# Performance work log

Hardware: AMD Instinct MI355X
Metric: run time of the kernel (lower is better)

## Reference

```python
import jax, jax.numpy as jnp
import numpy as np

TOP_K = 2
SCALING = 16.0 / 8.0  # alpha / rank


def setup_inputs() -> dict:
    key = jax.random.key(0)
    ks = jax.random.split(key, 9)
    B, V, D, P = 32, 21, 512, 64
    IN, OUT, E, R, H = D * P, 96, 8, 8, 256
    return {
        "x": jax.random.normal(ks[0], (B, V, D, P), jnp.float32),
        "W_base": jax.random.normal(ks[1], (OUT, IN), jnp.float32) * (IN ** -0.5),
        "b_base": jax.random.normal(ks[2], (OUT,), jnp.float32) * 0.01,
        "W1": jax.random.normal(ks[3], (H, D), jnp.float32) * (D ** -0.5),
        "b1": jax.random.normal(ks[4], (H,), jnp.float32) * 0.01,
        "W2": jax.random.normal(ks[5], (E, H), jnp.float32) * (H ** -0.5),
        "b2": jax.random.normal(ks[6], (E,), jnp.float32) * 0.01,
        "lora_A": jax.random.normal(ks[7], (E, R, IN), jnp.float32) * (IN ** -0.5),
        "lora_B": jax.random.normal(ks[8], (E, OUT, R), jnp.float32) * (R ** -0.5),
    }


def reference(x, W_base, b_base, W1, b1, W2, b2, lora_A, lora_B):
    B, V, D, P = x.shape
    E = lora_A.shape[0]
    # FlattenHead: flatten last two dims, then linear (dropout is identity in eval)
    flat = x.reshape(B, V, D * P)                      # [B, V, IN]
    base_out = flat @ W_base.T + b_base                # [B, V, OUT]
    # Router: pool over n_vars then patch dim -> [B, D]
    pooled = x.mean(axis=1).mean(axis=-1)
    h = jax.nn.relu(pooled @ W1.T + b1)
    logits = h @ W2.T + b2                             # [B, E]
    probs = jax.nn.softmax(logits, axis=-1)
    topw, topi = jax.lax.top_k(probs, TOP_K)           # [B, K]
    topw = topw / jnp.clip(topw.sum(-1, keepdims=True), 1e-6)
    # All LoRA experts (matches original dense compute), then weighted combine
    temp = jnp.einsum("bvi,eri->ebvr", flat, lora_A)   # [E, B, V, R]
    delta = jnp.einsum("ebvr,eor->ebvo", temp, lora_B) * SCALING  # [E, B, V, OUT]
    # Scatter top-k weights into dense [B, E] then combine (top-k sparse combine)
    w_full = jnp.zeros((B, E), x.dtype).at[jnp.arange(B)[:, None], topi].add(topw)
    moe_delta = jnp.einsum("be,ebvo->bvo", w_full, delta)
    return base_out + moe_delta, probs
```

## Files before the change

kernel.cpp:

```cpp
#include <hip/hip_runtime.h>

#define B_DIM 32
#define V_DIM 21
#define D_DIM 512
#define P_DIM 64
#define M_TOTAL 672
#define K_TOTAL 32768
#define OUT_DIM 96
#define E_DIM 8
#define R_DIM 8
#define H_DIM 256
#define N_TOTAL 160
#define SCALING 2.0f
#define POOL_SCALE (1.0f / (V_DIM * (float)P_DIM))

#define BM 64
#define BK 32
#define KSPLIT 64
#define K_PER_SPLIT (K_TOTAL / KSPLIT)
#define CHUNKS (K_PER_SPLIT / BK)
#define SMN (M_TOTAL * N_TOTAL)
#define RC_ROWS 2

typedef __attribute__((ext_vector_type(4))) float floatx4;
typedef __attribute__((ext_vector_type(8))) short short8;

__device__ __forceinline__ unsigned short f2bf(float f) {
  union { float f; unsigned int u; } v; v.f = f;
  unsigned int u = v.u + (0x7FFFu + ((v.u >> 16) & 1u));
  return (unsigned short)(u >> 16);
}

__device__ __forceinline__ unsigned int cvt_pk_bf16(float lo, float hi) {
  unsigned int r;
  asm("v_cvt_pk_bf16_f32 %0, %1, %2" : "=v"(r) : "v"(lo), "v"(hi));
  return r;
}

__device__ __forceinline__ void gl_lds16(const void* g, void* l) {
  __builtin_amdgcn_global_load_lds(
      (const __attribute__((address_space(1))) void*)g,
      (__attribute__((address_space(3))) void*)l, 16, 0, 0);
}

__global__ __launch_bounds__(256)
void convW_kernel(const float* __restrict__ W_base, const float* __restrict__ lora_A,
                  short* __restrict__ Wb, float* __restrict__ pooled) {
  int gid = blockIdx.x * 256 + threadIdx.x;
  if (blockIdx.x < 64) pooled[gid] = 0.0f;
  size_t base = (size_t)gid * 8;
  int row = (int)(base >> 15);
  int k = (int)(base & 32767);
  const float* src = (row < OUT_DIM) ? (W_base + ((size_t)row << 15) + k)
                                     : (lora_A + ((size_t)(row - OUT_DIM) << 15) + k);
  floatx4 v0 = ((const floatx4*)src)[0];
  floatx4 v1 = ((const floatx4*)src)[1];
  short8 sv;
  sv[0] = (short)f2bf(v0[0]); sv[1] = (short)f2bf(v0[1]);
  sv[2] = (short)f2bf(v0[2]); sv[3] = (short)f2bf(v0[3]);
  sv[4] = (short)f2bf(v1[0]); sv[5] = (short)f2bf(v1[1]);
  sv[6] = (short)f2bf(v1[2]); sv[7] = (short)f2bf(v1[3]);
  *(short8*)(Wb + base) = sv;
}

__global__ __launch_bounds__(256, 4)
void gemm_kernel(const float* __restrict__ x, const short* __restrict__ Wb,
                 float* __restrict__ P, float* __restrict__ pooled) {
  __shared__ __attribute__((aligned(16))) float ldsA[2][BM * BK];
  __shared__ __attribute__((aligned(16))) short ldsB[2][N_TOTAL * BK];
  __shared__ float lds_pool[5 * 8];

  const int tid = threadIdx.x;
  const int m0 = blockIdx.x * BM;
  const int ky = blockIdx.y;
  const int kbase = ky * K_PER_SPLIT;
  const int lane = tid & 63;
  const int wave = tid >> 6;
  const int quad = lane >> 4;
  const int l16 = lane & 15;
  const int b_first = m0 / V_DIM;
  const int d_first = kbase >> 6;

  if (tid < 40) lds_pool[tid] = 0.0f;

  const float* srcA[2];
  int dstA[2];
  #pragma unroll
  for (int it = 0; it < 2; ++it) {
    int idx = it * 256 + tid;
    int row = idx >> 3, j = idx & 7;
    int m = m0 + row; if (m > M_TOTAL - 1) m = M_TOTAL - 1;
    srcA[it] = x + (size_t)m * K_TOTAL + kbase + ((j ^ (row & 7)) << 2);
    dstA[it] = (it * 256 + (tid & 192)) << 2;
  }
  const short* srcB[3];
  int dstB[3];
  #pragma unroll
  for (int it = 0; it < 3; ++it) {
    int idx = it * 256 + tid;
    if (idx < 640) {
      int pair = idx >> 3, s8 = idx & 7;
      int c8 = s8 ^ (pair & 7);
      int row = pair * 2 + (c8 >> 2), j = c8 & 3;
      srcB[it] = Wb + (size_t)row * K_TOTAL + kbase + (j << 3);
      dstB[it] = (it * 256 + (tid & 192)) << 3;
    } else {
      srcB[it] = Wb; dstB[it] = 0;
    }
  }

  const int prow = tid >> 2;
  const int part = tid & 3;
  const int ps1 = (prow + part) & 7;
  const int ps2 = (ps1 + 4) & 7;
  const int pm = m0 + prow;
  const int pool_base = (pm < M_TOTAL) ? ((pm / V_DIM) - b_first) * 8 : -1;

#define ISSUE(c, bb)                                                          \
  {                                                                           \
    _Pragma("unroll")                                                         \
    for (int it = 0; it < 2; ++it)                                            \
      gl_lds16(srcA[it] + (c) * BK, &ldsA[bb][dstA[it]]);                     \
    _Pragma("unroll")                                                         \
    for (int it = 0; it < 2; ++it)                                            \
      gl_lds16(srcB[it] + (c) * BK, &ldsB[bb][dstB[it]]);                     \
    if (tid < 128) gl_lds16(srcB[2] + (c) * BK, &ldsB[bb][dstB[2]]);          \
  }

  floatx4 acc[10];
  #pragma unroll
  for (int nt = 0; nt < 10; ++nt) acc[nt] = (floatx4)(0.0f);

  ISSUE(0, 0);
  __syncthreads();

  #pragma unroll
  for (int c = 0; c < CHUNKS; ++c) {
    const int buf = c & 1;
    if (c + 1 < CHUNKS) ISSUE(c + 1, buf ^ 1);
    {
      const floatx4* aT = (const floatx4*)ldsA[buf];
      floatx4 u = aT[prow * 8 + ps1];
      floatx4 w = aT[prow * 8 + ps2];
      float s = ((u[0] + u[1]) + (u[2] + u[3])) + ((w[0] + w[1]) + (w[2] + w[3]));
      s += __shfl_down(s, 2, 4);
      s += __shfl_down(s, 1, 4);
      if (part == 0 && pool_base >= 0)
        atomicAdd(&lds_pool[pool_base + (c >> 1)], s);
    }
    {
      const floatx4* aT = (const floatx4*)ldsA[buf];
      const int r = wave * 16 + l16;
      floatx4 f0 = aT[r * 8 + ((2 * quad) ^ (r & 7))];
      floatx4 f1 = aT[r * 8 + ((2 * quad + 1) ^ (r & 7))];
      union { short8 s; unsigned int u[4]; } av;
      av.u[0] = cvt_pk_bf16(f0[0], f0[1]);
      av.u[1] = cvt_pk_bf16(f0[2], f0[3]);
      av.u[2] = cvt_pk_bf16(f1[0], f1[1]);
      av.u[3] = cvt_pk_bf16(f1[2], f1[3]);
      const short8* bT = (const short8*)ldsB[buf];
      #pragma unroll
      for (int nt = 0; nt < 10; ++nt) {
        int r2 = nt * 16 + l16;
        int pr = r2 >> 1;
        short8 b = bT[pr * 8 + ((((r2 & 1) << 2) | quad) ^ (pr & 7))];
        acc[nt] = __builtin_amdgcn_mfma_f32_16x16x32_bf16(av.s, b, acc[nt], 0, 0, 0);
      }
    }
    __syncthreads();
  }

  {
    const int mrow = m0 + wave * 16 + quad * 4;
    float* Pp = P + (size_t)ky * SMN + (size_t)mrow * N_TOTAL + l16;
    #pragma unroll
    for (int r = 0; r < 4; ++r)
      if (mrow + r < M_TOTAL)
        #pragma unroll
        for (int nt = 0; nt < 10; ++nt)
          Pp[(size_t)r * N_TOTAL + nt * 16] = acc[nt][r];
  }

  if (tid < 40) {
    int b = b_first + (tid >> 3);
    int d = d_first + (tid & 7);
    if (b < B_DIM)
      atomicAdd(&pooled[b * D_DIM + d], lds_pool[tid] * POOL_SCALE);
  }
}

__global__ __launch_bounds__(256)
void router_kernel(const float* __restrict__ pooled, const float* __restrict__ W1,
                   const float* __restrict__ b1, const float* __restrict__ W2,
                   const float* __restrict__ b2, float* __restrict__ wfull,
                   float* __restrict__ probs_out) {
  __shared__ float sp[D_DIM];
  __shared__ float sh[H_DIM];
  __shared__ float slog[E_DIM];
  const int b = blockIdx.x;
  const int t = threadIdx.x;
  sp[t] = pooled[b * D_DIM + t];
  sp[t + 256] = pooled[b * D_DIM + t + 256];
  __syncthreads();
  float acc = b1[t];
  const float* w1r = W1 + (size_t)t * D_DIM;
  for (int d = 0; d < D_DIM; ++d) acc += sp[d] * w1r[d];
  sh[t] = fmaxf(acc, 0.0f);
  __syncthreads();
  if (t < E_DIM) {
    float a = b2[t];
    const float* w2r = W2 + t * H_DIM;
    for (int j = 0; j < H_DIM; ++j) a += sh[j] * w2r[j];
    slog[t] = a;
  }
  __syncthreads();
  if (t == 0) {
    float p[E_DIM];
    float mx = slog[0];
    for (int e = 1; e < E_DIM; ++e) mx = fmaxf(mx, slog[e]);
    float se = 0.0f;
    for (int e = 0; e < E_DIM; ++e) { p[e] = __expf(slog[e] - mx); se += p[e]; }
    float inv = 1.0f / se;
    for (int e = 0; e < E_DIM; ++e) { p[e] *= inv; probs_out[b * E_DIM + e] = p[e]; }
    int i0 = 0;
    for (int e = 1; e < E_DIM; ++e) if (p[e] > p[i0]) i0 = e;
    int i1 = (i0 == 0) ? 1 : 0;
    for (int e = 0; e < E_DIM; ++e) if (e != i0 && p[e] > p[i1]) i1 = e;
    float s2 = p[i0] + p[i1];
    float invs = 1.0f / fmaxf(s2, 1e-6f);
    for (int e = 0; e < E_DIM; ++e) {
      float w = 0.0f;
      if (e == i0) w += p[i0] * invs;
      if (e == i1) w += p[i1] * invs;
      wfull[b * E_DIM + e] = w;
    }
  }
}

__global__ __launch_bounds__(256)
void reduce_combine_kernel(const float* __restrict__ P, const float* __restrict__ b_base,
                           const float* __restrict__ lora_B, const float* __restrict__ wfull,
                           float* __restrict__ out) {
  __shared__ float sS[RC_ROWS * N_TOTAL];
  const int t = threadIdx.x;
  const size_t base = (size_t)blockIdx.x * (RC_ROWS * N_TOTAL);
  for (int s = t; s < RC_ROWS * N_TOTAL; s += 256) {
    const float* Pp = P + base + s;
    float a = 0.0f;
    #pragma unroll 8
    for (int k = 0; k < KSPLIT; ++k) a += Pp[(size_t)k * SMN];
    sS[s] = a;
  }
  __syncthreads();
  if (t < RC_ROWS * OUT_DIM) {
    int mr = t / OUT_DIM;
    int o = t - mr * OUT_DIM;
    int mm = blockIdx.x * RC_ROWS + mr;
    int b = mm / V_DIM;
    const float* srow = sS + mr * N_TOTAL;
    float res = srow[o] + b_base[o];
    float moe = 0.0f;
    #pragma unroll
    for (int e = 0; e < E_DIM; ++e) {
      float we = wfull[b * E_DIM + e];
      if (we != 0.0f) {
        const float* lb = lora_B + ((size_t)e * OUT_DIM + o) * R_DIM;
        float dd = 0.0f;
        #pragma unroll
        for (int r = 0; r < R_DIM; ++r) dd += srow[OUT_DIM + e * R_DIM + r] * lb[r];
        moe += we * dd;
      }
    }
    out[(size_t)mm * OUT_DIM + o] = res + SCALING * moe;
  }
}

extern "C" void kernel_launch(void* const* d_in, const int* in_sizes, int n_in,
                              void* d_out, int out_size, void* d_ws, size_t ws_size,
                              hipStream_t stream) {
  const float* x      = (const float*)d_in[0];
  const float* W_base = (const float*)d_in[1];
  const float* b_base = (const float*)d_in[2];
  const float* W1     = (const float*)d_in[3];
  const float* b1     = (const float*)d_in[4];
  const float* W2     = (const float*)d_in[5];
  const float* b2     = (const float*)d_in[6];
  const float* lora_A = (const float*)d_in[7];
  const float* lora_B = (const float*)d_in[8];
  float* out = (float*)d_out;

  float* ws     = (float*)d_ws;
  float* pooled = ws;
  float* wfull  = ws + 16384;
  short* Wb     = (short*)(wfull + 256);
  float* P      = (float*)(Wb + (size_t)N_TOTAL * K_TOTAL);

  convW_kernel<<<(N_TOTAL * K_TOTAL / 8 + 255) / 256, 256, 0, stream>>>(
      W_base, lora_A, Wb, pooled);
  gemm_kernel<<<dim3(11, KSPLIT), 256, 0, stream>>>(x, Wb, P, pooled);
  router_kernel<<<B_DIM, 256, 0, stream>>>(pooled, W1, b1, W2, b2, wfull,
                                           out + (size_t)M_TOTAL * OUT_DIM);
  reduce_combine_kernel<<<M_TOTAL / RC_ROWS, 256, 0, stream>>>(
      P, b_base, lora_B, wfull, out);
}
```

Baseline: 206.1 us.

## Fuse weight bf16 conversion into GEMM, halve K-split, drop pooled atomics

Removes the separate weight-conversion kernel: the GEMM now loads fp32 W_base/lora_A rows into registers, converts them to bf16 and writes them to LDS after the MFMA work of each chunk. KSPLIT drops from 64 to 32, which halves the partial-sum buffer and the reduce traffic. Pooled sums are written as per-block partials and combined in the router instead of using global atomics, so no zeroing is needed. The reduce kernel is vectorised with float4 loads. The trade-offs are that each M-block now re-reads and re-converts fp32 weights (twice the bytes of the bf16 copy, repeated across 11 M-blocks), fewer GEMM blocks are launched, and register pressure rises.

```diff
diff --git a/kernel.cpp b/kernel.cpp
--- a/kernel.cpp
+++ b/kernel.cpp
@@ -16,20 +16,16 @@
 
 #define BM 64
 #define BK 32
-#define KSPLIT 64
+#define KSPLIT 32
 #define K_PER_SPLIT (K_TOTAL / KSPLIT)
 #define CHUNKS (K_PER_SPLIT / BK)
 #define SMN (M_TOTAL * N_TOTAL)
-#define RC_ROWS 2
+#define NMB 11
+#define RC_ROWS 4
 
 typedef __attribute__((ext_vector_type(4))) float floatx4;
 typedef __attribute__((ext_vector_type(8))) short short8;
-
-__device__ __forceinline__ unsigned short f2bf(float f) {
-  union { float f; unsigned int u; } v; v.f = f;
-  unsigned int u = v.u + (0x7FFFu + ((v.u >> 16) & 1u));
-  return (unsigned short)(u >> 16);
-}
+typedef __attribute__((ext_vector_type(2))) unsigned int uintx2;
 
 __device__ __forceinline__ unsigned int cvt_pk_bf16(float lo, float hi) {
   unsigned int r;
@@ -43,35 +39,17 @@
       (__attribute__((address_space(3))) void*)l, 16, 0, 0);
 }
 
-__global__ __launch_bounds__(256)
-void convW_kernel(const float* __restrict__ W_base, const float* __restrict__ lora_A,
-                  short* __restrict__ Wb, float* __restrict__ pooled) {
-  int gid = blockIdx.x * 256 + threadIdx.x;
-  if (blockIdx.x < 64) pooled[gid] = 0.0f;
-  size_t base = (size_t)gid * 8;
-  int row = (int)(base >> 15);
-  int k = (int)(base & 32767);
-  const float* src = (row < OUT_DIM) ? (W_base + ((size_t)row << 15) + k)
-                                     : (lora_A + ((size_t)(row - OUT_DIM) << 15) + k);
-  floatx4 v0 = ((const floatx4*)src)[0];
-  floatx4 v1 = ((const floatx4*)src)[1];
-  short8 sv;
-  sv[0] = (short)f2bf(v0[0]); sv[1] = (short)f2bf(v0[1]);
-  sv[2] = (short)f2bf(v0[2]); sv[3] = (short)f2bf(v0[3]);
-  sv[4] = (short)f2bf(v1[0]); sv[5] = (short)f2bf(v1[1]);
-  sv[6] = (short)f2bf(v1[2]); sv[7] = (short)f2bf(v1[3]);
-  *(short8*)(Wb + base) = sv;
-}
-
 __global__ __launch_bounds__(256, 4)
-void gemm_kernel(const float* __restrict__ x, const short* __restrict__ Wb,
-                 float* __restrict__ P, float* __restrict__ pooled) {
+void gemm_kernel(const float* __restrict__ x, const float* __restrict__ W_base,
+                 const float* __restrict__ lora_A, float* __restrict__ P,
+                 float* __restrict__ pp) {
   __shared__ __attribute__((aligned(16))) float ldsA[2][BM * BK];
   __shared__ __attribute__((aligned(16))) short ldsB[2][N_TOTAL * BK];
-  __shared__ float lds_pool[5 * 8];
+  __shared__ float lds_pool[5 * 16];
 
   const int tid = threadIdx.x;
-  const int m0 = blockIdx.x * BM;
+  const int mb = blockIdx.x;
+  const int m0 = mb * BM;
   const int ky = blockIdx.y;
   const int kbase = ky * K_PER_SPLIT;
   const int lane = tid & 63;
@@ -79,12 +57,11 @@
   const int quad = lane >> 4;
   const int l16 = lane & 15;
   const int b_first = m0 / V_DIM;
-  const int d_first = kbase >> 6;
-
-  if (tid < 40) lds_pool[tid] = 0.0f;
-
-  const float* srcA[2];
-  int dstA[2];
+  const int d_first = ky * (K_PER_SPLIT / P_DIM);
+
+  if (tid < 80) lds_pool[tid] = 0.0f;
+
+  const float* srcA[2]; int dstA[2];
   #pragma unroll
   for (int it = 0; it < 2; ++it) {
     int idx = it * 256 + tid;
@@ -93,20 +70,19 @@
     srcA[it] = x + (size_t)m * K_TOTAL + kbase + ((j ^ (row & 7)) << 2);
     dstA[it] = (it * 256 + (tid & 192)) << 2;
   }
-  const short* srcB[3];
-  int dstB[3];
+
+  const float* srcB[5]; int offB[5];
   #pragma unroll
-  for (int it = 0; it < 3; ++it) {
+  for (int it = 0; it < 5; ++it) {
     int idx = it * 256 + tid;
-    if (idx < 640) {
-      int pair = idx >> 3, s8 = idx & 7;
-      int c8 = s8 ^ (pair & 7);
-      int row = pair * 2 + (c8 >> 2), j = c8 & 3;
-      srcB[it] = Wb + (size_t)row * K_TOTAL + kbase + (j << 3);
-      dstB[it] = (it * 256 + (tid & 192)) << 3;
-    } else {
-      srcB[it] = Wb; dstB[it] = 0;
-    }
+    int row = idx >> 3, j = idx & 7;
+    const float* wrow = (row < OUT_DIM)
+        ? (W_base + (size_t)row * K_TOTAL)
+        : (lora_A + (size_t)(row - OUT_DIM) * K_TOTAL);
+    srcB[it] = wrow + kbase + (j << 2);
+    int p = row >> 1;
+    int c8 = ((row & 1) << 2) | (j >> 1);
+    offB[it] = p * 64 + ((c8 ^ (p & 7)) << 3) + ((j & 1) << 2);
   }
 
   const int prow = tid >> 2;
@@ -114,30 +90,37 @@
   const int ps1 = (prow + part) & 7;
   const int ps2 = (ps1 + 4) & 7;
   const int pm = m0 + prow;
-  const int pool_base = (pm < M_TOTAL) ? ((pm / V_DIM) - b_first) * 8 : -1;
-
-#define ISSUE(c, bb)                                                          \
-  {                                                                           \
-    _Pragma("unroll")                                                         \
-    for (int it = 0; it < 2; ++it)                                            \
-      gl_lds16(srcA[it] + (c) * BK, &ldsA[bb][dstA[it]]);                     \
-    _Pragma("unroll")                                                         \
-    for (int it = 0; it < 2; ++it)                                            \
-      gl_lds16(srcB[it] + (c) * BK, &ldsB[bb][dstB[it]]);                     \
-    if (tid < 128) gl_lds16(srcB[2] + (c) * BK, &ldsB[bb][dstB[2]]);          \
-  }
-
+  const int pool_base = (pm < M_TOTAL) ? ((pm / V_DIM) - b_first) * 16 : -1;
+
+  floatx4 rb[5];
   floatx4 acc[10];
   #pragma unroll
   for (int nt = 0; nt < 10; ++nt) acc[nt] = (floatx4)(0.0f);
 
-  ISSUE(0, 0);
-  __syncthreads();
-
-  #pragma unroll
+#define BLOAD(c)                                                              \
+  { _Pragma("unroll")                                                         \
+    for (int it = 0; it < 5; ++it)                                            \
+      rb[it] = *(const floatx4*)(srcB[it] + (c) * BK); }
+#define AISSUE(c, bb)                                                         \
+  { _Pragma("unroll")                                                         \
+    for (int it = 0; it < 2; ++it)                                            \
+      gl_lds16(srcA[it] + (c) * BK, &ldsA[bb][dstA[it]]); }
+#define BWRITE(bb)                                                            \
+  { _Pragma("unroll")                                                         \
+    for (int it = 0; it < 5; ++it) {                                          \
+      uintx2 w;                                                               \
+      w[0] = cvt_pk_bf16(rb[it][0], rb[it][1]);                               \
+      w[1] = cvt_pk_bf16(rb[it][2], rb[it][3]);                               \
+      *(uintx2*)&ldsB[bb][offB[it]] = w;                                      \
+    } }
+
+  BLOAD(0); AISSUE(0, 0); BWRITE(0);
+  __syncthreads();
+
+  #pragma unroll 2
   for (int c = 0; c < CHUNKS; ++c) {
     const int buf = c & 1;
-    if (c + 1 < CHUNKS) ISSUE(c + 1, buf ^ 1);
+    if (c + 1 < CHUNKS) { BLOAD(c + 1); AISSUE(c + 1, buf ^ 1); }
     {
       const floatx4* aT = (const floatx4*)ldsA[buf];
       floatx4 u = aT[prow * 8 + ps1];
@@ -167,6 +150,7 @@
         acc[nt] = __builtin_amdgcn_mfma_f32_16x16x32_bf16(av.s, b, acc[nt], 0, 0, 0);
       }
     }
+    if (c + 1 < CHUNKS) BWRITE(buf ^ 1);
     __syncthreads();
   }
 
@@ -181,16 +165,14 @@
           Pp[(size_t)r * N_TOTAL + nt * 16] = acc[nt][r];
   }
 
-  if (tid < 40) {
-    int b = b_first + (tid >> 3);
-    int d = d_first + (tid & 7);
-    if (b < B_DIM)
-      atomicAdd(&pooled[b * D_DIM + d], lds_pool[tid] * POOL_SCALE);
+  if (tid < 80) {
+    int bl = tid >> 4, dl = tid & 15;
+    pp[((size_t)(mb * 5 + bl)) * D_DIM + d_first + dl] = lds_pool[tid];
   }
 }
 
 __global__ __launch_bounds__(256)
-void router_kernel(const float* __restrict__ pooled, const float* __restrict__ W1,
+void router_kernel(const float* __restrict__ pp, const float* __restrict__ W1,
                    const float* __restrict__ b1, const float* __restrict__ W2,
                    const float* __restrict__ b2, float* __restrict__ wfull,
                    float* __restrict__ probs_out) {
@@ -199,8 +181,17 @@
   __shared__ float slog[E_DIM];
   const int b = blockIdx.x;
   const int t = threadIdx.x;
-  sp[t] = pooled[b * D_DIM + t];
-  sp[t + 256] = pooled[b * D_DIM + t + 256];
+  const int mb1 = (b * V_DIM) / BM;
+  const int mb2 = (b * V_DIM + V_DIM - 1) / BM;
+  const int bf1 = (mb1 * BM) / V_DIM;
+  const int bf2 = (mb2 * BM) / V_DIM;
+  const float* p1 = pp + (size_t)(mb1 * 5 + (b - bf1)) * D_DIM;
+  const float* p2 = pp + (size_t)(mb2 * 5 + (b - bf2)) * D_DIM;
+  for (int d = t; d < D_DIM; d += 256) {
+    float v = p1[d];
+    if (mb2 != mb1) v += p2[d];
+    sp[d] = v * POOL_SCALE;
+  }
   __syncthreads();
   float acc = b1[t];
   const float* w1r = W1 + (size_t)t * D_DIM;
@@ -243,18 +234,19 @@
                            float* __restrict__ out) {
   __shared__ float sS[RC_ROWS * N_TOTAL];
   const int t = threadIdx.x;
-  const size_t base = (size_t)blockIdx.x * (RC_ROWS * N_TOTAL);
-  for (int s = t; s < RC_ROWS * N_TOTAL; s += 256) {
-    const float* Pp = P + base + s;
-    float a = 0.0f;
+  const int NF4 = RC_ROWS * N_TOTAL / 4;
+  if (t < NF4) {
+    const floatx4* P4 = (const floatx4*)P;
+    size_t base = (size_t)blockIdx.x * NF4 + t;
+    floatx4 a = (floatx4)(0.0f);
     #pragma unroll 8
-    for (int k = 0; k < KSPLIT; ++k) a += Pp[(size_t)k * SMN];
-    sS[s] = a;
-  }
-  __syncthreads();
-  if (t < RC_ROWS * OUT_DIM) {
-    int mr = t / OUT_DIM;
-    int o = t - mr * OUT_DIM;
+    for (int k = 0; k < KSPLIT; ++k) a += P4[(size_t)k * (SMN / 4) + base];
+    *(floatx4*)&sS[t * 4] = a;
+  }
+  __syncthreads();
+  for (int i = t; i < RC_ROWS * OUT_DIM; i += 256) {
+    int mr = i / OUT_DIM;
+    int o = i - mr * OUT_DIM;
     int mm = blockIdx.x * RC_ROWS + mr;
     int b = mm / V_DIM;
     const float* srow = sS + mr * N_TOTAL;
@@ -289,16 +281,13 @@
   const float* lora_B = (const float*)d_in[8];
   float* out = (float*)d_out;
 
-  float* ws     = (float*)d_ws;
-  float* pooled = ws;
-  float* wfull  = ws + 16384;
-  short* Wb     = (short*)(wfull + 256);
-  float* P      = (float*)(Wb + (size_t)N_TOTAL * K_TOTAL);
-
-  convW_kernel<<<(N_TOTAL * K_TOTAL / 8 + 255) / 256, 256, 0, stream>>>(
-      W_base, lora_A, Wb, pooled);
-  gemm_kernel<<<dim3(11, KSPLIT), 256, 0, stream>>>(x, Wb, P, pooled);
-  router_kernel<<<B_DIM, 256, 0, stream>>>(pooled, W1, b1, W2, b2, wfull,
+  float* ws    = (float*)d_ws;
+  float* pp    = ws;
+  float* wfull = ws + NMB * 5 * D_DIM;
+  float* P     = wfull + 256;
+
+  gemm_kernel<<<dim3(NMB, KSPLIT), 256, 0, stream>>>(x, W_base, lora_A, P, pp);
+  router_kernel<<<B_DIM, 256, 0, stream>>>(pp, W1, b1, W2, b2, wfull,
                                            out + (size_t)M_TOTAL * OUT_DIM);
   reduce_combine_kernel<<<M_TOTAL / RC_ROWS, 256, 0, stream>>>(
       P, b_base, lora_B, wfull, out);
```

After: 216.9 us. 1.05x slower.
